# Kernel tuning notes

Measured on AMD Instinct MI355X. Metric: run time of the kernel, lower is better.

## Reference

```python
import jax, jax.numpy as jnp
import numpy as np

KERNEL_SIZE = 7       # NMS max-pool window
H, W = 512, 1024      # dims
TOP_K = 200
CIRCLE_RADIUS = 5
NUM_CLASSES = 34      # things are labelIds 24..33


def _circle_constants(radius):
    k = 2 * radius + 1
    ii, jj = np.meshgrid(np.arange(k), np.arange(k), indexing='ij')
    ox = (jj - radius).astype(np.float32)  # x offset of neighbor
    oy = (ii - radius).astype(np.float32)  # y offset of neighbor
    cd = np.sqrt(ox ** 2 + oy ** 2)
    cmask = (cd <= radius).astype(np.float32)
    n_pix = float(cmask.sum())
    thr = float((cd * cmask).sum() / n_pix)  # center_threshold buffer
    return ox, oy, cmask, n_pix, thr


def _vote_map(center_regressions, radius):
    # For each pixel p, average over circle neighbors q = p + o of ||o - reg(q)||
    # (get_patches with zero padding), then vote = -avg - 1.
    ox, oy, cmask, n_pix, thr = _circle_constants(radius)
    B, _, h, w = center_regressions.shape
    reg_p = jnp.pad(center_regressions, ((0, 0), (0, 0), (radius, radius), (radius, radius)))
    acc = jnp.zeros((B, h, w), center_regressions.dtype)
    k = 2 * radius + 1
    for i in range(k):          # fixed 11x11 window, ~97 in-circle taps
        for j in range(k):
            if cmask[i, j] == 0.0:
                continue
            rx = reg_p[:, 0, i:i + h, j:j + w]
            ry = reg_p[:, 1, i:i + h, j:j + w]
            acc = acc + jnp.sqrt((ox[i, j] - rx) ** 2 + (oy[i, j] - ry) ** 2)
    vote = -(acc / n_pix) - 1.0  # [B,H,W], always <= -1
    return vote, thr


def _forward(segmentation_logits, center_regressions):
    B = segmentation_logits.shape[0]
    seg_probs = jax.nn.softmax(segmentation_logits, axis=1)                # [B,C,H,W]
    seg_map = jnp.argmax(segmentation_logits, axis=1).astype(jnp.float32)  # [B,H,W]
    # Threshold(23.99, 50) then <= 33  <=>  23.99 < class <= 33
    things = (seg_map > 23.99) & (seg_map <= 33.0)
    # predicted absolute center per pixel; xy_coords are 1-based
    xg = jnp.arange(1, W + 1, dtype=jnp.float32)[None, None, :]
    yg = jnp.arange(1, H + 1, dtype=jnp.float32)[None, :, None]
    px = xg - center_regressions[:, 0]                                     # [B,H,W]
    py = yg - center_regressions[:, 1]
    vote, thr = _vote_map(center_regressions, CIRCLE_RADIUS)
    pooled = jax.lax.reduce_window(vote, -jnp.inf, jax.lax.max,
                                   (1, KERNEL_SIZE, KERNEL_SIZE), (1, 1, 1), 'SAME')
    keep = (pooled == vote) & (vote > -thr - 1.0)
    center_map = jnp.where(keep, vote, 0.0)                                # nms-ed vote map
    # top-k centers: surviving NMS positions ranked by aggregate vote value
    scores = jnp.where(center_map != 0.0, vote, -jnp.inf).reshape(B, -1)
    top_vals, top_idx = jax.lax.top_k(scores, TOP_K)                       # [B,K]
    ys = top_idx // W
    xs = top_idx % W
    valid = jnp.isfinite(top_vals)
    BIG = 1e9
    cx = jnp.where(valid, xs.astype(jnp.float32), BIG)
    cy = jnp.where(valid, ys.astype(jnp.float32), BIG)
    # nearest-center assignment; squared distance (argmin invariant under sqrt)
    d2 = (px[..., None] - cx[:, None, None, :]) ** 2 + (py[..., None] - cy[:, None, None, :]) ** 2
    inst_map = (jnp.argmin(d2, axis=-1).astype(jnp.int32) + 1) * things.astype(jnp.int32)
    return seg_probs, seg_map, center_map, inst_map, ys, xs, top_vals


def _instance_stats(inst_map, seg_map, seg_probs):
    # separate_inst_maps: per instance -> majority seg class, mean prob of that
    # class over the instance mask, and pixel count (vectorized via segment_sum)
    B = inst_map.shape[0]
    seg_ids = seg_map.astype(jnp.int32).reshape(B, -1)                     # [B,HW]
    inst_flat = inst_map.reshape(B, -1)                                    # [B,HW], 0 = background
    onehot = jax.nn.one_hot(seg_ids, NUM_CLASSES, dtype=jnp.float32)       # [B,HW,C]
    probs = jnp.transpose(seg_probs, (0, 2, 3, 1)).reshape(B, -1, NUM_CLASSES)
    seg_counts = jax.vmap(lambda v, s: jax.ops.segment_sum(v, s, num_segments=TOP_K + 1))(onehot, inst_flat)
    prob_sums = jax.vmap(lambda v, s: jax.ops.segment_sum(v, s, num_segments=TOP_K + 1))(probs, inst_flat)
    seg_counts = seg_counts[:, 1:]                                         # drop background -> [B,K,C]
    prob_sums = prob_sums[:, 1:]
    inst_size = seg_counts.sum(-1)                                         # [B,K]
    inst_class = jnp.argmax(seg_counts, axis=-1).astype(jnp.int32)         # [B,K]
    sel = jnp.take_along_axis(prob_sums, inst_class[..., None], axis=-1)[..., 0]
    inst_seg_prob = sel / jnp.maximum(inst_size, 1.0)
    return inst_class, inst_seg_prob, inst_size.astype(jnp.int32)


def setup_inputs() -> dict:
    key = jax.random.key(0)
    k1, k2, k3 = jax.random.split(key, 3)
    return {
        'segmentation_logits': jax.random.normal(k1, (2, NUM_CLASSES, H, W), jnp.float32),
        'center_maps_placeholder': jax.random.normal(k2, (2, 1, H, W), jnp.float32),
        'center_regressions': jax.random.normal(k3, (2, 2, H, W), jnp.float32),
    }


def reference(segmentation_logits, center_maps_placeholder, center_regressions):
    seg_probs, seg_map, center_map, inst_map, ys, xs, top_vals = _forward(
        segmentation_logits, center_regressions)
    inst_class, inst_seg_prob, inst_size = _instance_stats(inst_map, seg_map, seg_probs)
    centers = jnp.stack([ys, xs], -1).astype(jnp.int32)  # (row, col) like torch.nonzero
    return (inst_map, seg_map, centers, top_vals, inst_class, inst_seg_prob, inst_size, center_map)
```

## Files before the change

kernel.cpp:

```cpp
#include <hip/hip_runtime.h>
#include <cfloat>
#include <cmath>

#define NB 2
#define NC 34
#define NH 512
#define NW 1024
#define HWSZ (NH*NW)
#define TK 200
#define CAPC 49152
#define ACH 1024
#define ZWORDS (8 + NB*TK*NC + NB*TK)

#define PST 1040
#define RPROWS 522
#define RPLEFT 8
#define VPROWS 518
#define VPLEFT 4
#define RPSZ (RPROWS*PST)
#define VPSZ (VPROWS*PST)

typedef unsigned long long u64;

__global__ __launch_bounds__(256) void k_seg(const float* __restrict__ logits,
                                             const float* __restrict__ reg,
                                             float* __restrict__ segmap_out,
                                             float* __restrict__ mArr,
                                             float* __restrict__ dArr,
                                             float* __restrict__ reg_pad,
                                             float* __restrict__ vote_pad,
                                             int* __restrict__ zreg) {
    int p = blockIdx.x * 256 + threadIdx.x;
    if (p < ZWORDS) zreg[p] = 0;
    for (int t = p; t < NB * 2 * RPSZ; t += NB * HWSZ) {
        int c = t % PST;
        int rest = t / PST;
        int r = rest % RPROWS;
        int bc = rest / RPROWS;
        int rr = r - 5, cc = c - RPLEFT;
        float v = 0.f;
        if (rr >= 0 && rr < NH && cc >= 0 && cc < NW)
            v = reg[(size_t)bc * HWSZ + rr * NW + cc];
        reg_pad[t] = v;
    }
    for (int t = p; t < NB * VPSZ; t += NB * HWSZ) vote_pad[t] = -INFINITY;
    if (p >= NB * HWSZ) return;
    int b = p >> 19;
    int pix = p & (HWSZ - 1);
    const float* base = logits + (size_t)b * NC * HWSZ + pix;
    float v[NC];
#pragma unroll
    for (int c = 0; c < NC; c++) v[c] = base[(size_t)c * HWSZ];
    float m = -FLT_MAX; int bc = 0;
#pragma unroll
    for (int c = 0; c < NC; c++) { if (v[c] > m) { m = v[c]; bc = c; } }
    float den = 0.f;
#pragma unroll
    for (int c = 0; c < NC; c++) den += expf(v[c] - m);
    segmap_out[p] = (float)bc;
    mArr[p] = m;
    dArr[p] = den;
}

#define GETC(f, idx) (((idx)&3)==0 ? f[(idx)>>2].x : ((idx)&3)==1 ? f[(idx)>>2].y : \
                      ((idx)&3)==2 ? f[(idx)>>2].z : f[(idx)>>2].w)

__global__ __launch_bounds__(256, 4) void k_vote(const float* __restrict__ reg_pad,
                                                 float* __restrict__ vote_pad) {
    int tid = threadIdx.x;
    int blk = blockIdx.x;
    int b = blk >> 9;
    int q = blk & 511;
    int y = ((q & 7) << 6) | (q >> 3);
    int xb = tid << 2;
    const float* rp0 = reg_pad + (size_t)(b * 2 + 0) * RPSZ;
    const float* rp1 = reg_pad + (size_t)(b * 2 + 1) * RPSZ;
    float a0 = 0.f, a1 = 0.f, a2 = 0.f, a3 = 0.f;

    float4 fA0[5], fA1[5], fB0[5], fB1[5];

    auto loadwin = [&](int i, float4* f0, float4* f1) {
        const float* p0 = rp0 + (size_t)(y + i) * PST + xb;
        const float* p1 = rp1 + (size_t)(y + i) * PST + xb;
#pragma unroll
        for (int t = 0; t < 5; t++) f0[t] = *(const float4*)(p0 + 4 * t);
#pragma unroll
        for (int t = 0; t < 5; t++) f1[t] = *(const float4*)(p1 + 4 * t);
    };

    auto compute = [&](int i, const float4* f0, const float4* f1) {
        int d = i - 5;
        int ad = d < 0 ? -d : d;
        int w = (int)sqrtf((float)(25 - ad * ad));
        int lo = 5 - w, hi = 5 + w;
        float di = (float)d;
#pragma unroll
        for (int j = 0; j < 11; j++) {
            if (j < lo || j > hi) continue;
            float dj = (float)(j - 5);
            float dx, dy, ss;
            dx = __fsub_rn(dj, GETC(f0, j+3)); dy = __fsub_rn(di, GETC(f1, j+3));
            ss = __fadd_rn(__fmul_rn(dx,dx), __fmul_rn(dy,dy));
            a0 = __fadd_rn(a0, sqrtf(ss));
            dx = __fsub_rn(dj, GETC(f0, j+4)); dy = __fsub_rn(di, GETC(f1, j+4));
            ss = __fadd_rn(__fmul_rn(dx,dx), __fmul_rn(dy,dy));
            a1 = __fadd_rn(a1, sqrtf(ss));
            dx = __fsub_rn(dj, GETC(f0, j+5)); dy = __fsub_rn(di, GETC(f1, j+5));
            ss = __fadd_rn(__fmul_rn(dx,dx), __fmul_rn(dy,dy));
            a2 = __fadd_rn(a2, sqrtf(ss));
            dx = __fsub_rn(dj, GETC(f0, j+6)); dy = __fsub_rn(di, GETC(f1, j+6));
            ss = __fadd_rn(__fmul_rn(dx,dx), __fmul_rn(dy,dy));
            a3 = __fadd_rn(a3, sqrtf(ss));
        }
    };

    loadwin(0, fA0, fA1);
#pragma unroll 1
    for (int i = 0; i < 10; i += 2) {
        loadwin(i + 1, fB0, fB1);
        compute(i, fA0, fA1);
        loadwin(i + 2, fA0, fA1);
        compute(i + 1, fB0, fB1);
    }
    compute(10, fA0, fA1);

    float4 vv;
    vv.x = __fsub_rn(-__fdiv_rn(a0, 81.0f), 1.0f);
    vv.y = __fsub_rn(-__fdiv_rn(a1, 81.0f), 1.0f);
    vv.z = __fsub_rn(-__fdiv_rn(a2, 81.0f), 1.0f);
    vv.w = __fsub_rn(-__fdiv_rn(a3, 81.0f), 1.0f);
    *(float4*)(vote_pad + (size_t)b * VPSZ + (size_t)(y + 3) * PST + (xb + VPLEFT)) = vv;
}

__global__ __launch_bounds__(256) void k_pool(const float* __restrict__ vote_pad,
                                              float* __restrict__ cmap_out,
                                              u64* __restrict__ keys,
                                              int* __restrict__ ccnt,
                                              float thr_keep) {
    int tid = threadIdx.x;
    int blk = blockIdx.x;
    int b = blk >> 9;
    int q = blk & 511;
    int y = ((q & 7) << 6) | (q >> 3);
    int xb = tid << 2;
    const float* vp = vote_pad + (size_t)b * VPSZ;
    float cm[10];
#pragma unroll
    for (int t = 0; t < 10; t++) cm[t] = -INFINITY;
    float vv[4];
#pragma unroll 1
    for (int dy = -3; dy <= 3; dy++) {
        const float* row = vp + (size_t)(y + dy + 3) * PST + xb;
        float4 A = *(const float4*)(row);
        float4 Bq = *(const float4*)(row + 4);
        float4 Cq = *(const float4*)(row + 8);
        float L[12] = {A.x,A.y,A.z,A.w, Bq.x,Bq.y,Bq.z,Bq.w, Cq.x,Cq.y,Cq.z,Cq.w};
#pragma unroll
        for (int t = 0; t < 10; t++) cm[t] = fmaxf(cm[t], L[t + 1]);
        if (dy == 0) { vv[0]=L[4]; vv[1]=L[5]; vv[2]=L[6]; vv[3]=L[7]; }
    }
    int pix = y * NW + xb;
    float cmap[4];
#pragma unroll
    for (int k = 0; k < 4; k++) {
        float mx = cm[k];
#pragma unroll
        for (int u = 1; u < 7; u++) mx = fmaxf(mx, cm[k+u]);
        bool keep = (mx == vv[k]) && (vv[k] > thr_keep);
        cmap[k] = keep ? vv[k] : 0.0f;
        if (keep) {
            int pos = atomicAdd(&ccnt[b], 1);
            if (pos < CAPC) {
                unsigned u = __float_as_uint(vv[k]);
                unsigned ou = ((int)u < 0) ? ~u : (u | 0x80000000u);
                keys[(size_t)b * CAPC + pos] = ((u64)ou << 19) | (u64)(HWSZ - 1 - (pix + k));
            }
        }
    }
    *(float4*)(cmap_out + b * HWSZ + pix) = make_float4(cmap[0],cmap[1],cmap[2],cmap[3]);
}

__device__ inline void bitonic_desc(u64* a, int np2, int tid, int T) {
    for (int k = 2; k <= np2; k <<= 1) {
        for (int j = k >> 1; j > 0; j >>= 1) {
            for (int i = tid; i < np2; i += T) {
                int ixj = i ^ j;
                if (ixj > i) {
                    u64 x = a[i], y = a[ixj];
                    bool up = ((i & k) == 0);
                    if (up ? (x < y) : (x > y)) { a[i] = y; a[ixj] = x; }
                }
            }
            __syncthreads();
        }
    }
}

__global__ __launch_bounds__(1024) void k_topk(const u64* __restrict__ keys_g,
                                               const int* __restrict__ ccnt,
                                               float* __restrict__ cxArr,
                                               float* __restrict__ cyArr,
                                               float* __restrict__ out_centers,
                                               float* __restrict__ out_topvals) {
    __shared__ u64 sel[256];
    __shared__ int sred[16];
    __shared__ int scnt;
    const int T = 1024;
    int b = blockIdx.x;
    int tid = threadIdx.x;
    int lane = tid & 63;
    int wid = tid >> 6;
    int n = ccnt[b];
    if (n > CAPC) n = CAPC;
    const u64* Kg = keys_g + (size_t)b * CAPC;

    u64 thr = 0;
    for (int bit = 50; bit >= 0; --bit) {
        u64 cand = thr | (1ULL << bit);
        int c = 0;
        for (int i = tid; i < n; i += T) c += (Kg[i] >= cand) ? 1 : 0;
#pragma unroll
        for (int off = 32; off >= 1; off >>= 1) c += __shfl_down(c, off);
        if (lane == 0) sred[wid] = c;
        __syncthreads();
        int tot = 0;
#pragma unroll
        for (int w = 0; w < 16; w++) tot += sred[w];
        if (tot >= TK) thr = cand;
        __syncthreads();
    }
    if (tid == 0) scnt = 0;
    if (tid < 256) sel[tid] = 0;
    __syncthreads();
    for (int i = tid; i < n; i += T) {
        u64 k = Kg[i];
        if (k >= thr && k != 0ULL) {
            int p = atomicAdd(&scnt, 1);
            if (p < 256) sel[p] = k;
        }
    }
    __syncthreads();
    bitonic_desc(sel, 256, tid, T);
    if (tid < TK) {
        u64 w = sel[tid];
        bool valid = (w != 0ULL);
        unsigned ou = (unsigned)(w >> 19);
        unsigned ub = (ou & 0x80000000u) ? (ou & 0x7FFFFFFFu) : ~ou;
        float v = __uint_as_float(ub);
        int pix = valid ? (int)(HWSZ - 1 - (int)(w & 0x7FFFFULL)) : 0x7fffffff;
        int ys = pix >> 10;
        int xs = pix & (NW - 1);
        cxArr[b * TK + tid] = valid ? (float)xs : 1e9f;
        cyArr[b * TK + tid] = valid ? (float)ys : 1e9f;
        out_centers[(b * TK + tid) * 2 + 0] = (float)ys;
        out_centers[(b * TK + tid) * 2 + 1] = (float)xs;
        out_topvals[b * TK + tid] = valid ? v : -INFINITY;
    }
}

__global__ __launch_bounds__(256) void k_assign(const float* __restrict__ reg,
                                                const float* __restrict__ segmap,
                                                const float* __restrict__ cxArr,
                                                const float* __restrict__ cyArr,
                                                float* __restrict__ out_inst,
                                                int* __restrict__ segcnt) {
    __shared__ int lcnt[TK * NC];
    __shared__ float swx[TK];
    __shared__ float swy[TK];
    __shared__ int swk[TK];
    __shared__ float sred[256];
    __shared__ int wcnt[4];
    __shared__ float sbox[4];

    int tid = threadIdx.x;
    int bid = blockIdx.x;
    int b = bid >> 9;
    int r = bid & 511;
    int ty = r >> 5, tx = r & 31;
    int y0 = ty << 5, x0 = tx << 5;
    int row = tid >> 3;
    int col = (tid & 7) << 2;
    int y = y0 + row;
    int x = x0 + col;
    int pix0 = (y << 10) + x;

    for (int t = tid; t < TK * NC; t += 256) lcnt[t] = 0;

    const float* r0 = reg + (size_t)b * 2 * HWSZ;
    const float* r1 = r0 + HWSZ;
    float4 rx = *(const float4*)(r0 + pix0);
    float4 ry = *(const float4*)(r1 + pix0);
    float px[4], py[4];
    px[0] = __fsub_rn((float)(x + 1), rx.x); py[0] = __fsub_rn((float)(y + 1), ry.x);
    px[1] = __fsub_rn((float)(x + 2), rx.y); py[1] = __fsub_rn((float)(y + 1), ry.y);
    px[2] = __fsub_rn((float)(x + 3), rx.z); py[2] = __fsub_rn((float)(y + 1), ry.z);
    px[3] = __fsub_rn((float)(x + 4), rx.w); py[3] = __fsub_rn((float)(y + 1), ry.w);

    float pxlo = fminf(fminf(px[0], px[1]), fminf(px[2], px[3]));
    float pxhi = fmaxf(fmaxf(px[0], px[1]), fmaxf(px[2], px[3]));
    float pylo = fminf(fminf(py[0], py[1]), fminf(py[2], py[3]));
    float pyhi = fmaxf(fmaxf(py[0], py[1]), fmaxf(py[2], py[3]));
#pragma unroll
    for (int off = 32; off >= 1; off >>= 1) {
        pxlo = fminf(pxlo, __shfl_xor(pxlo, off));
        pxhi = fmaxf(pxhi, __shfl_xor(pxhi, off));
        pylo = fminf(pylo, __shfl_xor(pylo, off));
        pyhi = fmaxf(pyhi, __shfl_xor(pyhi, off));
    }
    int wid = tid >> 6;
    int lane = tid & 63;
    if (lane == 0) {
        sred[wid * 4 + 0] = pxlo; sred[wid * 4 + 1] = pxhi;
        sred[wid * 4 + 2] = pylo; sred[wid * 4 + 3] = pyhi;
    }
    __syncthreads();
    if (tid == 0) {
        float a = sred[0], bq = sred[1], c = sred[2], d = sred[3];
        for (int w = 1; w < 4; w++) {
            a  = fminf(a,  sred[w * 4 + 0]);
            bq = fmaxf(bq, sred[w * 4 + 1]);
            c  = fminf(c,  sred[w * 4 + 2]);
            d  = fmaxf(d,  sred[w * 4 + 3]);
        }
        sbox[0] = a; sbox[1] = bq; sbox[2] = c; sbox[3] = d;
    }
    __syncthreads();
    float bxlo = sbox[0], bxhi = sbox[1], bylo = sbox[2], byhi = sbox[3];

    float Lk = 0.f, Uk = INFINITY, cxv = 0.f, cyv = 0.f;
    if (tid < TK) {
        cxv = cxArr[b * TK + tid];
        cyv = cyArr[b * TK + tid];
        float dl = fmaxf(fmaxf(__fsub_rn(bxlo, cxv), __fsub_rn(cxv, bxhi)), 0.f);
        float el = fmaxf(fmaxf(__fsub_rn(bylo, cyv), __fsub_rn(cyv, byhi)), 0.f);
        float du = fmaxf(__fsub_rn(cxv, bxlo), __fsub_rn(bxhi, cxv));
        float eu = fmaxf(__fsub_rn(cyv, bylo), __fsub_rn(byhi, cyv));
        Lk = __fadd_rn(__fmul_rn(dl, dl), __fmul_rn(el, el));
        Uk = __fadd_rn(__fmul_rn(du, du), __fmul_rn(eu, eu));
    }
    sred[tid] = Uk;
    __syncthreads();
#pragma unroll
    for (int s = 128; s > 0; s >>= 1) {
        if (tid < s) sred[tid] = fminf(sred[tid], sred[tid + s]);
        __syncthreads();
    }
    float Umin = sred[0];

    bool flag = (tid < TK) && (Lk <= Umin);
    u64 mask = __ballot(flag);
    int wpre = __popcll(mask & ((1ULL << lane) - 1ULL));
    if (lane == 0) wcnt[wid] = (int)__popcll(mask);
    __syncthreads();
    int base_off = 0;
#pragma unroll
    for (int w = 0; w < 4; w++) if (w < wid) base_off += wcnt[w];
    int m = wcnt[0] + wcnt[1] + wcnt[2] + wcnt[3];
    if (flag) {
        int p = base_off + wpre;
        swx[p] = cxv; swy[p] = cyv; swk[p] = tid;
    }
    __syncthreads();

    float bd[4]; int bk[4];
#pragma unroll
    for (int it = 0; it < 4; it++) { bd[it] = INFINITY; bk[it] = 0; }
    for (int k2 = 0; k2 < m; k2++) {
        float cx = swx[k2];
        float cy = swy[k2];
        int kk = swk[k2];
#pragma unroll
        for (int it = 0; it < 4; it++) {
            float dx = __fsub_rn(px[it], cx);
            float dy = __fsub_rn(py[it], cy);
            float d2 = __fadd_rn(__fmul_rn(dx, dx), __fmul_rn(dy, dy));
            if (d2 < bd[it]) { bd[it] = d2; bk[it] = kk; }
        }
    }

    float4 sm = *(const float4*)(segmap + (size_t)b * HWSZ + pix0);
    float scls[4] = {sm.x, sm.y, sm.z, sm.w};
    float oi[4];
#pragma unroll
    for (int it = 0; it < 4; it++) {
        int cls = (int)scls[it];
        int thing = (cls >= 24) ? 1 : 0;
        int inst = (bk[it] + 1) * thing;
        oi[it] = (float)inst;
        if (inst) atomicAdd(&lcnt[bk[it] * NC + cls], 1);
    }
    *(float4*)(out_inst + (size_t)b * HWSZ + pix0) = make_float4(oi[0], oi[1], oi[2], oi[3]);
    __syncthreads();
    for (int t = tid; t < TK * NC; t += 256) {
        int v = lcnt[t];
        if (v) atomicAdd(&segcnt[b * TK * NC + t], v);
    }
}

__global__ __launch_bounds__(256) void k_stats(const int* __restrict__ segcnt,
                                               float* __restrict__ out_icls,
                                               float* __restrict__ out_isize,
                                               float* __restrict__ out_iprob,
                                               int* __restrict__ icls,
                                               int* __restrict__ isize) {
    int t = blockIdx.x * 256 + threadIdx.x;
    if (t >= NB * TK) return;
    const int* row = segcnt + (size_t)t * NC;
    int total = 0; int bc = 0; int bv = -1;
#pragma unroll
    for (int c = 0; c < NC; c++) {
        int v = row[c];
        total += v;
        if (v > bv) { bv = v; bc = c; }
    }
    out_icls[t] = (float)bc;
    out_isize[t] = (float)total;
    out_iprob[t] = 0.f;
    icls[t] = bc;
    isize[t] = total;
}

__global__ __launch_bounds__(256) void k_probsum(const float* __restrict__ logits,
                                                 const float* __restrict__ inst_f,
                                                 const float* __restrict__ mArr,
                                                 const float* __restrict__ dArr,
                                                 const int* __restrict__ icls,
                                                 const int* __restrict__ isize,
                                                 float* __restrict__ out_iprob) {
    __shared__ float lps[TK];
    int tid = threadIdx.x;
    int base = blockIdx.x * ACH;
    int b = base >> 19;
    for (int t = tid; t < TK; t += 256) lps[t] = 0.f;
    __syncthreads();
    int p0 = base + tid * 4;
    float4 fi = *(const float4*)(inst_f + p0);
    float4 fm = *(const float4*)(mArr + p0);
    float4 fd = *(const float4*)(dArr + p0);
    float insts[4] = {fi.x, fi.y, fi.z, fi.w};
    float ms[4] = {fm.x, fm.y, fm.z, fm.w};
    float ds[4] = {fd.x, fd.y, fd.z, fd.w};
#pragma unroll
    for (int it = 0; it < 4; it++) {
        int inst = (int)insts[it];
        if (inst) {
            int p = p0 + it;
            int pix = p & (HWSZ - 1);
            int c = icls[b * TK + inst - 1];
            float xv = logits[(size_t)(b * NC + c) * HWSZ + pix];
            float pr = __fdiv_rn(expf(__fsub_rn(xv, ms[it])), ds[it]);
            atomicAdd(&lps[inst - 1], pr);
        }
    }
    __syncthreads();
    for (int t = tid; t < TK; t += 256) {
        float s = lps[t];
        if (s != 0.f) {
            float sz = fmaxf((float)isize[b * TK + t], 1.0f);
            atomicAdd(&out_iprob[b * TK + t], s / sz);
        }
    }
}

static float compute_thr_keep() {
    float cdm[121];
    int t = 0;
    for (int i = 0; i < 11; i++) {
        for (int j = 0; j < 11; j++) {
            float ox = (float)(j - 5), oy = (float)(i - 5);
            float cd = sqrtf(ox * ox + oy * oy);
            float cm = (cd <= 5.0f) ? 1.0f : 0.0f;
            cdm[t++] = cd * cm;
        }
    }
    float r[8];
    for (int k = 0; k < 8; k++) r[k] = cdm[k];
    int i = 8;
    for (; i < 121 - (121 % 8); i += 8)
        for (int k = 0; k < 8; k++) r[k] += cdm[i + k];
    float res = ((r[0] + r[1]) + (r[2] + r[3])) + ((r[4] + r[5]) + (r[6] + r[7]));
    for (; i < 121; i++) res += cdm[i];
    float thr = res / 81.0f;
    double kt = -(double)thr - 1.0;
    return (float)kt;
}

extern "C" void kernel_launch(void* const* d_in, const int* in_sizes, int n_in,
                              void* d_out, int out_size, void* d_ws, size_t ws_size,
                              hipStream_t stream) {
    const float* logits = (const float*)d_in[0];
    const float* reg    = (const float*)d_in[2];
    float* out = (float*)d_out;

    float* o_inst    = out;
    float* o_seg     = out + 1048576;
    float* o_centers = out + 2097152;
    float* o_topvals = out + 2097952;
    float* o_icls    = out + 2098352;
    float* o_iprob   = out + 2098752;
    float* o_isize   = out + 2099152;
    float* o_cmap    = out + 2099552;

    u64* keys = (u64*)d_ws;
    float* wsf = (float*)(keys + (size_t)NB * CAPC);
    size_t o = 0;
    int*   zreg    = (int*)(wsf + o); o += ZWORDS;
    int*   ccnt    = zreg;
    int*   segcnt  = zreg + 8;
    float* reg_pad = wsf + o; o += (size_t)NB * 2 * RPSZ;
    float* vote_pad= wsf + o; o += (size_t)NB * VPSZ;
    float* mArr    = wsf + o; o += (size_t)NB * HWSZ;
    float* dArr    = wsf + o; o += (size_t)NB * HWSZ;
    float* cxArr   = wsf + o; o += NB * TK;
    float* cyArr   = wsf + o; o += NB * TK;
    int*   icls    = (int*)(wsf + o); o += NB * TK;
    int*   isize   = (int*)(wsf + o); o += NB * TK;

    float thr_keep = compute_thr_keep();

    int gridPix = (NB * HWSZ) / 256;
    int gridRow = NB * NH;
    int gridAgg = (NB * HWSZ) / ACH;

    k_seg<<<gridPix, 256, 0, stream>>>(logits, reg, o_seg, mArr, dArr, reg_pad, vote_pad, zreg);
    k_vote<<<gridRow, 256, 0, stream>>>(reg_pad, vote_pad);
    k_pool<<<gridRow, 256, 0, stream>>>(vote_pad, o_cmap, keys, ccnt, thr_keep);
    k_topk<<<NB, 1024, 0, stream>>>(keys, ccnt, cxArr, cyArr, o_centers, o_topvals);
    k_assign<<<gridAgg, 256, 0, stream>>>(reg, o_seg, cxArr, cyArr, o_inst, segcnt);
    k_stats<<<(NB * TK + 255) / 256, 256, 0, stream>>>(segcnt, o_icls, o_isize, o_iprob, icls, isize);
    k_probsum<<<gridAgg, 256, 0, stream>>>(logits, o_inst, mArr, dArr, icls, isize, o_iprob);
}
```

Before: 404.2 us.

## Fuse seg softmax into vote kernel, radix-select top-k, shrink class histograms

The per-pixel argmax/softmax stats move into the vote kernel, using float4 loads, and a new row-wise prep kernel does the padding and zeroing with vectorised copies. The 51-pass bitwise threshold search in top-k becomes a multi-level 11-bit histogram radix select, which reads the candidate keys far fewer times. Per-instance class counts now track only the 10 thing classes instead of 34, and the stats kernel is folded into the prob-sum kernel so one launch goes away. The risks are a heavier, register-hungry vote kernel, redundant stats recomputation in every block, and the class-0 fallback when an instance is empty.

```diff
diff --git a/kernel.cpp b/kernel.cpp
--- a/kernel.cpp
+++ b/kernel.cpp
@@ -10,7 +10,8 @@
 #define TK 200
 #define CAPC 49152
 #define ACH 1024
-#define ZWORDS (8 + NB*TK*NC + NB*TK)
+#define NTH 10
+#define ZWORDS (8 + NB*TK*NTH)
 
 #define PST 1040
 #define RPROWS 522
@@ -22,51 +23,50 @@
 
 typedef unsigned long long u64;
 
-__global__ __launch_bounds__(256) void k_seg(const float* __restrict__ logits,
-                                             const float* __restrict__ reg,
-                                             float* __restrict__ segmap_out,
-                                             float* __restrict__ mArr,
-                                             float* __restrict__ dArr,
-                                             float* __restrict__ reg_pad,
-                                             float* __restrict__ vote_pad,
-                                             int* __restrict__ zreg) {
-    int p = blockIdx.x * 256 + threadIdx.x;
-    if (p < ZWORDS) zreg[p] = 0;
-    for (int t = p; t < NB * 2 * RPSZ; t += NB * HWSZ) {
-        int c = t % PST;
-        int rest = t / PST;
-        int r = rest % RPROWS;
-        int bc = rest / RPROWS;
-        int rr = r - 5, cc = c - RPLEFT;
-        float v = 0.f;
-        if (rr >= 0 && rr < NH && cc >= 0 && cc < NW)
-            v = reg[(size_t)bc * HWSZ + rr * NW + cc];
-        reg_pad[t] = v;
-    }
-    for (int t = p; t < NB * VPSZ; t += NB * HWSZ) vote_pad[t] = -INFINITY;
-    if (p >= NB * HWSZ) return;
-    int b = p >> 19;
-    int pix = p & (HWSZ - 1);
-    const float* base = logits + (size_t)b * NC * HWSZ + pix;
-    float v[NC];
-#pragma unroll
-    for (int c = 0; c < NC; c++) v[c] = base[(size_t)c * HWSZ];
-    float m = -FLT_MAX; int bc = 0;
-#pragma unroll
-    for (int c = 0; c < NC; c++) { if (v[c] > m) { m = v[c]; bc = c; } }
-    float den = 0.f;
-#pragma unroll
-    for (int c = 0; c < NC; c++) den += expf(v[c] - m);
-    segmap_out[p] = (float)bc;
-    mArr[p] = m;
-    dArr[p] = den;
+#define PREP_ROWB (NB*2*RPROWS)
+#define PREP_VF4 ((NB*VPSZ)/4)
+#define PREP_VB ((PREP_VF4 + 255)/256)
+#define PREP_ZB ((ZWORDS + NB*TK + 255)/256 + 1)
+__global__ __launch_bounds__(256) void k_prep(const float* __restrict__ reg,
+                                              float* __restrict__ reg_pad,
+                                              float* __restrict__ vote_pad,
+                                              int* __restrict__ zreg,
+                                              float* __restrict__ o_iprob) {
+    int bid = blockIdx.x;
+    int tid = threadIdx.x;
+    if (bid < PREP_ROWB) {
+        int bc = bid / RPROWS;
+        int r = bid % RPROWS;
+        float* dst = reg_pad + (size_t)bc * RPSZ + (size_t)r * PST;
+        if (r >= 5 && r < 517) {
+            const float* src = reg + (size_t)bc * HWSZ + (size_t)(r - 5) * NW;
+            *(float4*)(dst + RPLEFT + 4 * tid) = *(const float4*)(src + 4 * tid);
+            if (tid < 2) *(float4*)(dst + 4 * tid) = make_float4(0.f, 0.f, 0.f, 0.f);
+            else if (tid < 4) *(float4*)(dst + 1032 + 4 * (tid - 2)) = make_float4(0.f, 0.f, 0.f, 0.f);
+        } else {
+            for (int i = tid; i < PST / 4; i += 256)
+                *(float4*)(dst + 4 * i) = make_float4(0.f, 0.f, 0.f, 0.f);
+        }
+    } else if (bid < PREP_ROWB + PREP_VB) {
+        int idx4 = (bid - PREP_ROWB) * 256 + tid;
+        if (idx4 < PREP_VF4)
+            *(float4*)(vote_pad + (size_t)idx4 * 4) = make_float4(-INFINITY, -INFINITY, -INFINITY, -INFINITY);
+    } else {
+        int z = (bid - (PREP_ROWB + PREP_VB)) * 256 + tid;
+        if (z < ZWORDS) zreg[z] = 0;
+        else if (z < ZWORDS + NB * TK) o_iprob[z - ZWORDS] = 0.f;
+    }
 }
 
 #define GETC(f, idx) (((idx)&3)==0 ? f[(idx)>>2].x : ((idx)&3)==1 ? f[(idx)>>2].y : \
                       ((idx)&3)==2 ? f[(idx)>>2].z : f[(idx)>>2].w)
 
-__global__ __launch_bounds__(256, 4) void k_vote(const float* __restrict__ reg_pad,
-                                                 float* __restrict__ vote_pad) {
+__global__ __launch_bounds__(256, 4) void k_vote_seg(const float* __restrict__ reg_pad,
+                                                     float* __restrict__ vote_pad,
+                                                     const float* __restrict__ logits,
+                                                     float* __restrict__ segmap_out,
+                                                     float* __restrict__ mArr,
+                                                     float* __restrict__ dArr) {
     int tid = threadIdx.x;
     int blk = blockIdx.x;
     int b = blk >> 9;
@@ -130,6 +130,31 @@
     vv.z = __fsub_rn(-__fdiv_rn(a2, 81.0f), 1.0f);
     vv.w = __fsub_rn(-__fdiv_rn(a3, 81.0f), 1.0f);
     *(float4*)(vote_pad + (size_t)b * VPSZ + (size_t)(y + 3) * PST + (xb + VPLEFT)) = vv;
+
+    const float* lg = logits + (size_t)b * NC * HWSZ + (size_t)y * NW + xb;
+    float4 m4 = make_float4(-FLT_MAX, -FLT_MAX, -FLT_MAX, -FLT_MAX);
+    float4 bc4 = make_float4(0.f, 0.f, 0.f, 0.f);
+#pragma unroll
+    for (int c = 0; c < NC; c++) {
+        float4 v = *(const float4*)(lg + (size_t)c * HWSZ);
+        if (v.x > m4.x) { m4.x = v.x; bc4.x = (float)c; }
+        if (v.y > m4.y) { m4.y = v.y; bc4.y = (float)c; }
+        if (v.z > m4.z) { m4.z = v.z; bc4.z = (float)c; }
+        if (v.w > m4.w) { m4.w = v.w; bc4.w = (float)c; }
+    }
+    float4 den = make_float4(0.f, 0.f, 0.f, 0.f);
+#pragma unroll
+    for (int c = 0; c < NC; c++) {
+        float4 v = *(const float4*)(lg + (size_t)c * HWSZ);
+        den.x += expf(v.x - m4.x);
+        den.y += expf(v.y - m4.y);
+        den.z += expf(v.z - m4.z);
+        den.w += expf(v.w - m4.w);
+    }
+    size_t po = (size_t)b * HWSZ + (size_t)y * NW + xb;
+    *(float4*)(segmap_out + po) = bc4;
+    *(float4*)(mArr + po) = m4;
+    *(float4*)(dArr + po) = den;
 }
 
 __global__ __launch_bounds__(256) void k_pool(const float* __restrict__ vote_pad,
@@ -202,33 +227,81 @@
                                                float* __restrict__ cyArr,
                                                float* __restrict__ out_centers,
                                                float* __restrict__ out_topvals) {
+    __shared__ int hist[2048];
+    __shared__ int ssum[1024];
     __shared__ u64 sel[256];
-    __shared__ int sred[16];
     __shared__ int scnt;
+    __shared__ int sB, sSab, scB;
     const int T = 1024;
     int b = blockIdx.x;
     int tid = threadIdx.x;
-    int lane = tid & 63;
-    int wid = tid >> 6;
     int n = ccnt[b];
     if (n > CAPC) n = CAPC;
     const u64* Kg = keys_g + (size_t)b * CAPC;
 
-    u64 thr = 0;
-    for (int bit = 50; bit >= 0; --bit) {
-        u64 cand = thr | (1ULL << bit);
-        int c = 0;
-        for (int i = tid; i < n; i += T) c += (Kg[i] >= cand) ? 1 : 0;
-#pragma unroll
-        for (int off = 32; off >= 1; off >>= 1) c += __shfl_down(c, off);
-        if (lane == 0) sred[wid] = c;
-        __syncthreads();
-        int tot = 0;
-#pragma unroll
-        for (int w = 0; w < 16; w++) tot += sred[w];
-        if (tot >= TK) thr = cand;
-        __syncthreads();
-    }
+    u64 thr;
+    if (n <= TK) {
+        thr = 1;
+    } else {
+        u64 prefixval = 0;
+        int pbits = 0, need = TK;
+        thr = 0;
+        const int widths[5] = {11, 11, 11, 11, 7};
+        bool done = false;
+        for (int lvl = 0; lvl < 5 && !done; ++lvl) {
+            int w = widths[lvl];
+            int nb = 1 << w;
+            int shift = 51 - pbits - w;
+            for (int i = tid; i < nb; i += T) hist[i] = 0;
+            __syncthreads();
+            for (int i = tid; i < n; i += T) {
+                u64 k = Kg[i];
+                if ((k >> (51 - pbits)) == prefixval)
+                    atomicAdd(&hist[(int)((k >> shift) & (u64)(nb - 1))], 1);
+            }
+            __syncthreads();
+            int items = (nb + T - 1) / T;
+            int sv = 0;
+            for (int it = 0; it < items; ++it) {
+                int j = tid * items + it;
+                if (j < nb) sv += hist[j];
+            }
+            ssum[tid] = sv;
+            __syncthreads();
+            for (int off = 1; off < T; off <<= 1) {
+                int v = (tid + off < T) ? ssum[tid + off] : 0;
+                __syncthreads();
+                ssum[tid] += v;
+                __syncthreads();
+            }
+            int incl = ssum[tid];
+            int excl = (tid + 1 < T) ? ssum[tid + 1] : 0;
+            if (excl < need && need <= incl) {
+                int acc = excl;
+                int base2 = tid * items;
+                for (int it = items - 1; it >= 0; --it) {
+                    int j = base2 + it;
+                    if (j >= nb) continue;
+                    int h = hist[j];
+                    if (acc + h >= need) { sB = j; sSab = acc; scB = h; break; }
+                    acc += h;
+                }
+            }
+            __syncthreads();
+            int B = sB, Sab = sSab, cB = scB;
+            int sel_total = (TK - need) + Sab;
+            if (sel_total + cB <= 256) {
+                thr = ((prefixval << w) | (u64)B) << shift;
+                done = true;
+            } else {
+                prefixval = (prefixval << w) | (u64)B;
+                pbits += w;
+                need = need - Sab;
+            }
+            __syncthreads();
+        }
+    }
+
     if (tid == 0) scnt = 0;
     if (tid < 256) sel[tid] = 0;
     __syncthreads();
@@ -264,7 +337,7 @@
                                                 const float* __restrict__ cyArr,
                                                 float* __restrict__ out_inst,
                                                 int* __restrict__ segcnt) {
-    __shared__ int lcnt[TK * NC];
+    __shared__ int lcnt[TK * NTH];
     __shared__ float swx[TK];
     __shared__ float swy[TK];
     __shared__ int swk[TK];
@@ -284,7 +357,7 @@
     int x = x0 + col;
     int pix0 = (y << 10) + x;
 
-    for (int t = tid; t < TK * NC; t += 256) lcnt[t] = 0;
+    for (int t = tid; t < TK * NTH; t += 256) lcnt[t] = 0;
 
     const float* r0 = reg + (size_t)b * 2 * HWSZ;
     const float* r1 = r0 + HWSZ;
@@ -387,50 +460,47 @@
         int thing = (cls >= 24) ? 1 : 0;
         int inst = (bk[it] + 1) * thing;
         oi[it] = (float)inst;
-        if (inst) atomicAdd(&lcnt[bk[it] * NC + cls], 1);
+        if (inst) atomicAdd(&lcnt[bk[it] * NTH + (cls - 24)], 1);
     }
     *(float4*)(out_inst + (size_t)b * HWSZ + pix0) = make_float4(oi[0], oi[1], oi[2], oi[3]);
     __syncthreads();
-    for (int t = tid; t < TK * NC; t += 256) {
+    for (int t = tid; t < TK * NTH; t += 256) {
         int v = lcnt[t];
-        if (v) atomicAdd(&segcnt[b * TK * NC + t], v);
-    }
-}
-
-__global__ __launch_bounds__(256) void k_stats(const int* __restrict__ segcnt,
-                                               float* __restrict__ out_icls,
-                                               float* __restrict__ out_isize,
-                                               float* __restrict__ out_iprob,
-                                               int* __restrict__ icls,
-                                               int* __restrict__ isize) {
-    int t = blockIdx.x * 256 + threadIdx.x;
-    if (t >= NB * TK) return;
-    const int* row = segcnt + (size_t)t * NC;
-    int total = 0; int bc = 0; int bv = -1;
-#pragma unroll
-    for (int c = 0; c < NC; c++) {
-        int v = row[c];
-        total += v;
-        if (v > bv) { bv = v; bc = c; }
-    }
-    out_icls[t] = (float)bc;
-    out_isize[t] = (float)total;
-    out_iprob[t] = 0.f;
-    icls[t] = bc;
-    isize[t] = total;
-}
-
-__global__ __launch_bounds__(256) void k_probsum(const float* __restrict__ logits,
-                                                 const float* __restrict__ inst_f,
-                                                 const float* __restrict__ mArr,
-                                                 const float* __restrict__ dArr,
-                                                 const int* __restrict__ icls,
-                                                 const int* __restrict__ isize,
-                                                 float* __restrict__ out_iprob) {
+        if (v) atomicAdd(&segcnt[b * TK * NTH + t], v);
+    }
+}
+
+__global__ __launch_bounds__(256) void k_statsprob(const float* __restrict__ logits,
+                                                   const float* __restrict__ inst_f,
+                                                   const float* __restrict__ mArr,
+                                                   const float* __restrict__ dArr,
+                                                   const int* __restrict__ segcnt,
+                                                   float* __restrict__ out_icls,
+                                                   float* __restrict__ out_isize,
+                                                   float* __restrict__ out_iprob) {
     __shared__ float lps[TK];
+    __shared__ int sicls[TK];
+    __shared__ float ssz[TK];
     int tid = threadIdx.x;
     int base = blockIdx.x * ACH;
     int b = base >> 19;
+    if (tid < TK) {
+        const int* rowp = segcnt + (size_t)(b * TK + tid) * NTH;
+        int total = 0, bc = 0, bv = -1;
+#pragma unroll
+        for (int c = 0; c < NTH; c++) {
+            int v = rowp[c];
+            total += v;
+            if (v > bv) { bv = v; bc = c; }
+        }
+        int cls = (total == 0) ? 0 : (24 + bc);
+        sicls[tid] = cls;
+        ssz[tid] = fmaxf((float)total, 1.0f);
+        if ((blockIdx.x & 511) == 0) {
+            out_icls[b * TK + tid] = (float)cls;
+            out_isize[b * TK + tid] = (float)total;
+        }
+    }
     for (int t = tid; t < TK; t += 256) lps[t] = 0.f;
     __syncthreads();
     int p0 = base + tid * 4;
@@ -446,7 +516,7 @@
         if (inst) {
             int p = p0 + it;
             int pix = p & (HWSZ - 1);
-            int c = icls[b * TK + inst - 1];
+            int c = sicls[inst - 1];
             float xv = logits[(size_t)(b * NC + c) * HWSZ + pix];
             float pr = __fdiv_rn(expf(__fsub_rn(xv, ms[it])), ds[it]);
             atomicAdd(&lps[inst - 1], pr);
@@ -456,7 +526,7 @@
     for (int t = tid; t < TK; t += 256) {
         float s = lps[t];
         if (s != 0.f) {
-            float sz = fmaxf((float)isize[b * TK + t], 1.0f);
+            float sz = ssz[t];
             atomicAdd(&out_iprob[b * TK + t], s / sz);
         }
     }
@@ -513,20 +583,17 @@
     float* dArr    = wsf + o; o += (size_t)NB * HWSZ;
     float* cxArr   = wsf + o; o += NB * TK;
     float* cyArr   = wsf + o; o += NB * TK;
-    int*   icls    = (int*)(wsf + o); o += NB * TK;
-    int*   isize   = (int*)(wsf + o); o += NB * TK;
 
     float thr_keep = compute_thr_keep();
 
-    int gridPix = (NB * HWSZ) / 256;
+    int gridPrep = PREP_ROWB + PREP_VB + PREP_ZB;
     int gridRow = NB * NH;
     int gridAgg = (NB * HWSZ) / ACH;
 
-    k_seg<<<gridPix, 256, 0, stream>>>(logits, reg, o_seg, mArr, dArr, reg_pad, vote_pad, zreg);
-    k_vote<<<gridRow, 256, 0, stream>>>(reg_pad, vote_pad);
+    k_prep<<<gridPrep, 256, 0, stream>>>(reg, reg_pad, vote_pad, zreg, o_iprob);
+    k_vote_seg<<<gridRow, 256, 0, stream>>>(reg_pad, vote_pad, logits, o_seg, mArr, dArr);
     k_pool<<<gridRow, 256, 0, stream>>>(vote_pad, o_cmap, keys, ccnt, thr_keep);
     k_topk<<<NB, 1024, 0, stream>>>(keys, ccnt, cxArr, cyArr, o_centers, o_topvals);
     k_assign<<<gridAgg, 256, 0, stream>>>(reg, o_seg, cxArr, cyArr, o_inst, segcnt);
-    k_stats<<<(NB * TK + 255) / 256, 256, 0, stream>>>(segcnt, o_icls, o_isize, o_iprob, icls, isize);
-    k_probsum<<<gridAgg, 256, 0, stream>>>(logits, o_inst, mArr, dArr, icls, isize, o_iprob);
-}
+    k_statsprob<<<gridAgg, 256, 0, stream>>>(logits, o_inst, mArr, dArr, segcnt, o_icls, o_isize, o_iprob);
+}
```

Measured after the change: 379.7 us. 1.06x faster.
